# Performance work log

Measured on AMD Instinct MI355X. Metric: run time of the kernel, lower is better.

The kernel has to match this reference:

```python
import jax, jax.numpy as jnp
import numpy as np

N_NODES = 50000   # gnn_nodes_num
N_EDGES = 800000  # avg degree 16
HIDDEN = 64       # hidden_channels
BATCH_Y = 2048    # |y|


def setup_inputs() -> dict:
    key = jax.random.key(0)
    ks = jax.random.split(key, 16)
    s = 0.05
    H = HIDDEN
    return {
        "x": jnp.arange(N_NODES, dtype=jnp.int32),
        "edge_index": jax.random.randint(ks[0], (2, N_EDGES), 0, N_NODES, dtype=jnp.int32),
        "y": jax.random.randint(ks[1], (BATCH_Y,), 0, N_NODES, dtype=jnp.int32),
        # learned params
        "emb": jax.random.normal(ks[2], (N_NODES, H), dtype=jnp.float32) * s,
        "Wq": jax.random.normal(ks[3], (H, H), dtype=jnp.float32) * s,
        "bq": jnp.zeros((H,), dtype=jnp.float32),
        "Wk": jax.random.normal(ks[4], (H, H), dtype=jnp.float32) * s,
        "bk": jnp.zeros((H,), dtype=jnp.float32),
        "Wv": jax.random.normal(ks[5], (H, H), dtype=jnp.float32) * s,
        "bv": jnp.zeros((H,), dtype=jnp.float32),
        "Ws": jax.random.normal(ks[6], (H, H), dtype=jnp.float32) * s,  # root/skip lin
        "bs": jnp.zeros((H,), dtype=jnp.float32),
        "W1": jax.random.normal(ks[7], (H, N_NODES), dtype=jnp.float32) * s,
        "b1": jnp.zeros((N_NODES,), dtype=jnp.float32),
    }


def reference(x, edge_index, y, emb, Wq, bq, Wk, bk, Wv, bv, Ws, bs, W1, b1):
    H = Wq.shape[1]
    h = emb[x]                                  # [N, H] embedding lookup
    src, dst = edge_index[0], edge_index[1]

    # TransformerConv (heads=1, root_weight=True): per-node projections
    q = h @ Wq + bq                             # [N, H]
    k = h @ Wk + bk
    v = h @ Wv + bv

    # attention logits per edge, softmax grouped by destination node
    logits = jnp.sum(q[dst] * k[src], axis=-1) / jnp.sqrt(jnp.float32(H))  # [E]
    m = jax.ops.segment_max(logits, dst, num_segments=N_NODES)             # [N]
    e = jnp.exp(logits - m[dst])
    denom = jax.ops.segment_sum(e, dst, num_segments=N_NODES)              # [N]
    alpha = e / denom[dst]                                                 # [E]

    agg = jax.ops.segment_sum(alpha[:, None] * v[src], dst, num_segments=N_NODES)
    out = agg + h @ Ws + bs                     # [N, H] GAT output

    # for each node u: sum of out[dst] over edges with src == u  (vectorized
    # form of the original per-y boolean-mask loop), then gather at y
    neigh = jax.ops.segment_sum(out[dst], src, num_segments=N_NODES)       # [N, H]
    new_x = neigh[y]                            # [B, H]

    return jax.nn.softmax(new_x @ W1 + b1, axis=-1)  # [B, N]
```

## Files before the change

kernel.cpp:

```cpp
#include <hip/hip_runtime.h>
#include <math.h>

#define NN 50000
#define NE 800000
#define HH 64
#define NB 2048
#define NPAD 53248
#define NST3 52
#define TPS3 16
#define LOG2E 1.4426950408889634f
#define HBLK 3125
#define QBLK 782

typedef __attribute__((ext_vector_type(8))) short bf16x8;
typedef __attribute__((ext_vector_type(4))) float f32x4;

__device__ inline ushort f2bf(float f) {
  uint u = __float_as_uint(f);
  uint r = (u + 0x7fffu + ((u >> 16) & 1u)) >> 16;
  return (ushort)r;
}
__device__ inline float bf2f(uint u) { return __uint_as_float(u << 16); }

__device__ inline float fexp2(float x) {
#if __has_builtin(__builtin_amdgcn_exp2f)
  return __builtin_amdgcn_exp2f(x);
#else
  return exp2f(x);
#endif
}

__global__ __launch_bounds__(256) void k_prep(
    const float* __restrict__ W1, const float* __restrict__ b1,
    const float* __restrict__ Wq, const float* __restrict__ Wk,
    const float* __restrict__ Wv, const float* __restrict__ Ws,
    ushort* __restrict__ w1p, float* __restrict__ eb, ushort* __restrict__ WT,
    int* cnt_d, int* cnt_s, char* flag, char* ymark)
{
  int i = blockIdx.x * 256 + threadIdx.x;
  if (i < NN) { cnt_d[i] = 0; cnt_s[i] = 0; flag[i] = 0; ymark[i] = 0; }
  if (i < 4 * HH * HH) {
    int m = i >> 12, rem = i & 4095;
    int c = rem >> 6, kk = rem & 63;
    const float* W = (m == 0) ? Wq : (m == 1) ? Wk : (m == 2) ? Wv : Ws;
    WT[i] = f2bf(W[kk * HH + c]);
  }
  if (i < NPAD) {
    eb[i] = (i < NN) ? __expf(b1[i]) : 0.f;
    uint4 o[8];
    ushort* op = (ushort*)o;
    if (i < NN) {
#pragma unroll
      for (int k = 0; k < HH; ++k) op[k] = f2bf(W1[(size_t)k * NN + i] * LOG2E);
    } else {
#pragma unroll
      for (int k = 0; k < HH; ++k) op[k] = 0;
    }
    int t = i >> 6, nt = (i >> 4) & 3, lr = i & 15;
    ushort* tp = w1p + (size_t)t * 4096;
#pragma unroll
    for (int kt = 0; kt < 2; ++kt)
#pragma unroll
      for (int lk = 0; lk < 4; ++lk)
        *(uint4*)(tp + (kt * 4 + nt) * 512 + (lk * 16 + lr) * 8) = o[kt * 4 + lk];
  }
}

__global__ __launch_bounds__(256) void k_mark(const int* __restrict__ y,
                                              char* __restrict__ ymark) {
  int i = blockIdx.x * 256 + threadIdx.x;
  if (i < NB) ymark[y[i]] = 1;
}

__global__ __launch_bounds__(256) void k_hq(
    const int* __restrict__ src, const int* __restrict__ dst,
    const char* __restrict__ ymark,
    int* cnt_s, int* cnt_d, char* __restrict__ flag,
    int* __restrict__ rank_d, int* __restrict__ rank_s,
    const int* __restrict__ x, const float* __restrict__ emb,
    const ushort* __restrict__ WT,
    const float* __restrict__ bq, const float* __restrict__ bk,
    const float* __restrict__ bv, const float* __restrict__ bs,
    ushort* __restrict__ qb, ushort* __restrict__ kb, ushort* __restrict__ vb,
    float* __restrict__ hs)
{
  if (blockIdx.x < HBLK) {
    int e = blockIdx.x * 256 + threadIdx.x;
    if (e < NE) {
      int s = src[e], d = dst[e];
      rank_d[e] = atomicAdd(&cnt_d[d], 1);
      if (ymark[s]) {
        rank_s[e] = atomicAdd(&cnt_s[s], 1);
        flag[d] = 1;
      } else {
        rank_s[e] = -1;
      }
    }
    return;
  }
  int l = threadIdx.x & 63, w = threadIdx.x >> 6;
  int lr = l & 15, lk = l >> 4;
  int r0 = (blockIdx.x - HBLK) * 64;
  const ushort* wt = WT + w * HH * HH;
  const float* B = (w == 0) ? bq : (w == 1) ? bk : (w == 2) ? bv : bs;

  bf16x8 b[2][4];
#pragma unroll
  for (int kt = 0; kt < 2; ++kt)
#pragma unroll
    for (int nt = 0; nt < 4; ++nt)
      b[kt][nt] = *(const bf16x8*)(wt + (nt * 16 + lr) * HH + kt * 32 + lk * 8);

  bf16x8 a[2][4];
#pragma unroll
  for (int mt = 0; mt < 4; ++mt) {
    int row = r0 + mt * 16 + lr;
    int g = (row < NN) ? x[row] : 0;
    const float* hp = emb + (size_t)g * HH;
#pragma unroll
    for (int kt = 0; kt < 2; ++kt) {
      float4 f0 = *(const float4*)(hp + kt * 32 + lk * 8);
      float4 f1 = *(const float4*)(hp + kt * 32 + lk * 8 + 4);
      bf16x8 af;
      af[0] = f2bf(f0.x); af[1] = f2bf(f0.y); af[2] = f2bf(f0.z); af[3] = f2bf(f0.w);
      af[4] = f2bf(f1.x); af[5] = f2bf(f1.y); af[6] = f2bf(f1.z); af[7] = f2bf(f1.w);
      a[kt][mt] = af;
    }
  }

  f32x4 acc[4][4];
  const f32x4 z4 = {0.f, 0.f, 0.f, 0.f};
#pragma unroll
  for (int mt = 0; mt < 4; ++mt)
#pragma unroll
    for (int nt = 0; nt < 4; ++nt) acc[mt][nt] = z4;
#pragma unroll
  for (int kt = 0; kt < 2; ++kt)
#pragma unroll
    for (int mt = 0; mt < 4; ++mt)
#pragma unroll
      for (int nt = 0; nt < 4; ++nt)
        acc[mt][nt] = __builtin_amdgcn_mfma_f32_16x16x32_bf16(a[kt][mt], b[kt][nt], acc[mt][nt], 0, 0, 0);

  if (w < 3) {
    ushort* Db = (w == 0) ? qb : (w == 1) ? kb : vb;
#pragma unroll
    for (int mt = 0; mt < 4; ++mt)
#pragma unroll
      for (int r = 0; r < 4; ++r) {
        int row = r0 + mt * 16 + lk * 4 + r;
        if (row < NN) {
#pragma unroll
          for (int nt = 0; nt < 4; ++nt) {
            int c = nt * 16 + lr;
            Db[(size_t)row * HH + c] = f2bf(acc[mt][nt][r] + B[c]);
          }
        }
      }
  } else {
#pragma unroll
    for (int mt = 0; mt < 4; ++mt)
#pragma unroll
      for (int r = 0; r < 4; ++r) {
        int row = r0 + mt * 16 + lk * 4 + r;
        if (row < NN) {
#pragma unroll
          for (int nt = 0; nt < 4; ++nt) {
            int c = nt * 16 + lr;
            hs[(size_t)row * HH + c] = acc[mt][nt][r] + B[c];
          }
        }
      }
  }
}

__global__ __launch_bounds__(1024) void k_scan(
    const int* __restrict__ cnt_d, int* indptr_d,
    const int* __restrict__ cnt_s, int* indptr_s)
{
  const int* cnt = (blockIdx.x == 0) ? cnt_d : cnt_s;
  int* indptr    = (blockIdx.x == 0) ? indptr_d : indptr_s;
  __shared__ int sums[1024];
  const int CH = (NN + 1023) / 1024;
  int t = threadIdx.x;
  int begin = t * CH;
  int end = begin + CH; if (end > NN) end = NN;
  int s = 0;
  for (int i = begin; i < end; ++i) s += cnt[i];
  sums[t] = s;
  __syncthreads();
  for (int off = 1; off < 1024; off <<= 1) {
    int val = (t >= off) ? sums[t - off] : 0;
    __syncthreads();
    sums[t] += val;
    __syncthreads();
  }
  int prefix = (t == 0) ? 0 : sums[t - 1];
  for (int i = begin; i < end; ++i) {
    indptr[i] = prefix;
    prefix += cnt[i];
  }
  if (t == 0) indptr[NN] = sums[1023];
}

__global__ __launch_bounds__(256) void k_efill(
    const int* __restrict__ src, const int* __restrict__ dst,
    const ushort* __restrict__ qb, const ushort* __restrict__ kb,
    const char* __restrict__ flag,
    const int* __restrict__ indptr_s, const int* __restrict__ indptr_d,
    const int* __restrict__ rank_d, const int* __restrict__ rank_s,
    int* __restrict__ dstlist_s, int2* __restrict__ slot_d)
{
  int gid = blockIdx.x * 256 + threadIdx.x;
  int e = gid >> 2;
  int lane = gid & 3;
  if (e >= NE) return;
  int s = src[e], d = dst[e];
  bool fd = flag[d];
  float p = 0.f;
  if (fd) {
    const uint4* qp = (const uint4*)(qb + (size_t)d * HH + lane * 16);
    const uint4* kp = (const uint4*)(kb + (size_t)s * HH + lane * 16);
    uint4 qa0 = qp[0], ka0 = kp[0];
    uint4 qa1 = qp[1], ka1 = kp[1];
    p += bf2f(qa0.x & 0xffffu) * bf2f(ka0.x & 0xffffu) + bf2f(qa0.x >> 16) * bf2f(ka0.x >> 16);
    p += bf2f(qa0.y & 0xffffu) * bf2f(ka0.y & 0xffffu) + bf2f(qa0.y >> 16) * bf2f(ka0.y >> 16);
    p += bf2f(qa0.z & 0xffffu) * bf2f(ka0.z & 0xffffu) + bf2f(qa0.z >> 16) * bf2f(ka0.z >> 16);
    p += bf2f(qa0.w & 0xffffu) * bf2f(ka0.w & 0xffffu) + bf2f(qa0.w >> 16) * bf2f(ka0.w >> 16);
    p += bf2f(qa1.x & 0xffffu) * bf2f(ka1.x & 0xffffu) + bf2f(qa1.x >> 16) * bf2f(ka1.x >> 16);
    p += bf2f(qa1.y & 0xffffu) * bf2f(ka1.y & 0xffffu) + bf2f(qa1.y >> 16) * bf2f(ka1.y >> 16);
    p += bf2f(qa1.z & 0xffffu) * bf2f(ka1.z & 0xffffu) + bf2f(qa1.z >> 16) * bf2f(ka1.z >> 16);
    p += bf2f(qa1.w & 0xffffu) * bf2f(ka1.w & 0xffffu) + bf2f(qa1.w >> 16) * bf2f(ka1.w >> 16);
    p += __shfl_xor(p, 2);
    p += __shfl_xor(p, 1);
  }
  if (lane == 0) {
    if (fd) {
      int pd = indptr_d[d] + rank_d[e];
      int2 sl; sl.x = s; sl.y = __float_as_int(p * (0.125f * LOG2E));
      slot_d[pd] = sl;
    }
    int rs = rank_s[e];
    if (rs >= 0) dstlist_s[indptr_s[s] + rs] = d;
  }
}

__global__ __launch_bounds__(256) void k_agg(
    const int* __restrict__ indptr_d, const int2* __restrict__ slot_d,
    const ushort* __restrict__ vb, const char* __restrict__ flag,
    float* __restrict__ hs)
{
  int w = (blockIdx.x * 256 + threadIdx.x) >> 6;
  int lane = threadIdx.x & 63;
  if (w >= NN) return;
  if (!flag[w]) return;
  int beg = indptr_d[w], end = indptr_d[w + 1];
  if (beg == end) return;
  float den0 = 0.f, den1 = 0.f, acc0 = 0.f, acc1 = 0.f;
  int j = beg;
  for (; j + 1 < end; j += 2) {
    int2 sa = slot_d[j];
    int2 sb = slot_d[j + 1];
    float pa = fexp2(__int_as_float(sa.y));
    float pb = fexp2(__int_as_float(sb.y));
    float va = bf2f((uint)vb[(size_t)sa.x * HH + lane]);
    float vc = bf2f((uint)vb[(size_t)sb.x * HH + lane]);
    den0 += pa; den1 += pb;
    acc0 = fmaf(pa, va, acc0);
    acc1 = fmaf(pb, vc, acc1);
  }
  if (j < end) {
    int2 sa = slot_d[j];
    float pa = fexp2(__int_as_float(sa.y));
    den0 += pa;
    acc0 = fmaf(pa, bf2f((uint)vb[(size_t)sa.x * HH + lane]), acc0);
  }
  hs[(size_t)w * HH + lane] += (acc0 + acc1) / (den0 + den1);
}

__global__ __launch_bounds__(256) void k_newx(
    const int* __restrict__ y, const int* __restrict__ indptr_s,
    const int* __restrict__ dstlist_s, const float* __restrict__ outn,
    ushort* __restrict__ nxbf)
{
  int w = (blockIdx.x * 256 + threadIdx.x) >> 6;
  int lane = threadIdx.x & 63;
  if (w >= NB) return;
  int u = y[w];
  int beg = indptr_s[u], end = indptr_s[u + 1];
  float acc = 0.f;
  for (int j = beg; j < end; ++j) acc += outn[(size_t)dstlist_s[j] * HH + lane];
  nxbf[w * HH + lane] = f2bf(acc);
}

#define LOADP(A, t) do { const ushort* tp_ = w1p + (size_t)(t) * 4096;           \
  _Pragma("unroll") for (int kt = 0; kt < 2; ++kt)                               \
  _Pragma("unroll") for (int nt = 0; nt < 4; ++nt)                               \
    A[kt][nt] = *(const bf16x8*)(tp_ + (kt * 4 + nt) * 512 + l * 8);             \
} while (0)

#define MFMA8(A, acc) do {                                                       \
  _Pragma("unroll") for (int kt = 0; kt < 2; ++kt)                               \
  _Pragma("unroll") for (int nt = 0; nt < 4; ++nt)                               \
    acc[nt] = __builtin_amdgcn_mfma_f32_16x16x32_bf16(A[kt][nt], bm[kt], acc[nt], 0, 0, 0); \
} while (0)

__global__ __launch_bounds__(256) void k_finZ(
    const ushort* __restrict__ nxbf, const ushort* __restrict__ w1p,
    const float* __restrict__ eb, ushort* __restrict__ zb,
    float* __restrict__ Spart)
{
  __shared__ ushort lt[4][16][512];
  int tid = threadIdx.x;
  int l = tid & 63, w = tid >> 6;
  int lr = l & 15, lk = l >> 4;
  int b = blockIdx.x;
  int st = b % NST3, rg = b / NST3;
  int r0 = rg * 64 + w * 16;
  int tile0 = st * TPS3;
  const f32x4 z4 = {0.f, 0.f, 0.f, 0.f};

  bf16x8 bm[2];
#pragma unroll
  for (int kt = 0; kt < 2; ++kt)
    bm[kt] = *(const bf16x8*)(nxbf + (size_t)(r0 + lr) * HH + kt * 32 + lk * 8);

  float se = 0.f;
#pragma unroll
  for (int s = 0; s < 2; ++s) {
#pragma unroll
    for (int t = 0; t < 8; ++t) {
      int tile = tile0 + s * 8 + t;
      bf16x8 A0[2][4];
      LOADP(A0, tile);
      f32x4 acc[4];
#pragma unroll
      for (int nt = 0; nt < 4; ++nt) acc[nt] = z4;
      MFMA8(A0, acc);
#pragma unroll
      for (int nt = 0; nt < 4; ++nt) {
        int n0 = tile * 64 + nt * 16 + lk * 4;
        f32x4 e4 = *(const f32x4*)(eb + n0);
        union { _Float16 h[4]; uint2 u; } pk;
#pragma unroll
        for (int r = 0; r < 4; ++r) {
          float ur = fexp2(acc[nt][r]) * e4[r];
          se += ur;
          pk.h[r] = (_Float16)ur;
        }
        int uL = t * 16 + nt * 4 + lk;
        int uP = uL ^ (2 * (lr & 7));
        *(uint2*)&lt[w][lr][uP * 4] = pk.u;
      }
    }
    int colbase = (tile0 + s * 8) * 64;
#pragma unroll
    for (int r = 0; r < 16; ++r) {
      uint4 v = *(const uint4*)&lt[w][r][(l ^ (r & 7)) * 8];
      *(uint4*)(zb + (size_t)(r0 + r) * NPAD + colbase + l * 8) = v;
    }
  }
  se += __shfl_xor(se, 16);
  se += __shfl_xor(se, 32);
  if (lk == 0) Spart[(r0 + lr) * NST3 + st] = se;
}

__global__ __launch_bounds__(256) void k_sinv(const float* __restrict__ Spart,
                                              float* __restrict__ Sinv) {
  int r = blockIdx.x * 256 + threadIdx.x;
  if (r < NB) {
    float s = 0.f;
#pragma unroll
    for (int j = 0; j < NST3; ++j) s += Spart[r * NST3 + j];
    Sinv[r] = 1.0f / s;
  }
}

__global__ __launch_bounds__(256) void k_finN(
    const ushort* __restrict__ zb, const float* __restrict__ Sinv,
    float* __restrict__ out)
{
  int r = blockIdx.x;
  float sv = Sinv[r];
  const ushort* zr = zb + (size_t)r * NPAD;
  float* orow = out + (size_t)r * NN;
  for (int c0 = threadIdx.x * 8; c0 < NN; c0 += 2048) {
    uint4 zv = *(const uint4*)(zr + c0);
    const _Float16* hp = (const _Float16*)&zv;
    f32x4 v0, v1;
#pragma unroll
    for (int j = 0; j < 4; ++j) {
      v0[j] = (float)hp[j] * sv;
      v1[j] = (float)hp[4 + j] * sv;
    }
    *(f32x4*)(orow + c0) = v0;
    *(f32x4*)(orow + c0 + 4) = v1;
  }
}

#define PROCA(A, t) do { int bn0_ = (t) * 64;                                    \
  f32x4 acc[4];                                                                  \
  _Pragma("unroll") for (int nt = 0; nt < 4; ++nt) acc[nt] = z4;                 \
  MFMA8(A, acc);                                                                 \
  _Pragma("unroll") for (int nt = 0; nt < 4; ++nt) {                             \
    int n0 = bn0_ + nt * 16 + lk * 4;                                            \
    f32x4 e4 = *(const f32x4*)(eb + n0);                                         \
    _Pragma("unroll") for (int r = 0; r < 4; ++r)                                \
      se += fexp2(acc[nt][r]) * e4[r];                                           \
  }                                                                              \
} while (0)

#define PROCB(A, t) do { int bn0_ = (t) * 64;                                    \
  f32x4 acc[4];                                                                  \
  _Pragma("unroll") for (int nt = 0; nt < 4; ++nt) acc[nt] = z4;                 \
  MFMA8(A, acc);                                                                 \
  _Pragma("unroll") for (int nt = 0; nt < 4; ++nt) {                             \
    int n0 = bn0_ + nt * 16 + lk * 4;                                            \
    f32x4 e4 = *(const f32x4*)(eb + n0);                                         \
    f32x4 vx;                                                                    \
    _Pragma("unroll") for (int r = 0; r < 4; ++r)                                \
      vx[r] = fexp2(acc[nt][r]) * e4[r] * sv;                                    \
    if (n0 < NN)                                                                 \
      __builtin_nontemporal_store(vx, (f32x4*)(out + (size_t)(r0 + lr) * NN + n0)); \
  }                                                                              \
} while (0)

__global__ __launch_bounds__(256, 4) void k_finA(
    const ushort* __restrict__ nxbf, const ushort* __restrict__ w1p,
    const float* __restrict__ eb, float* __restrict__ Spart)
{
  int tid = threadIdx.x;
  int l = tid & 63, w = tid >> 6;
  int lr = l & 15, lk = l >> 4;
  int b = blockIdx.x;
  int st = b % NST3, rg = b / NST3;
  int r0 = rg * 64 + w * 16;
  int tile0 = st * TPS3;
  const f32x4 z4 = {0.f, 0.f, 0.f, 0.f};
  bf16x8 bm[2];
#pragma unroll
  for (int kt = 0; kt < 2; ++kt)
    bm[kt] = *(const bf16x8*)(nxbf + (size_t)(r0 + lr) * HH + kt * 32 + lk * 8);
  float se = 0.f;
  {
    bf16x8 A0[2][4];
#pragma unroll
    for (int t = 0; t < TPS3; ++t) { LOADP(A0, tile0 + t); PROCA(A0, tile0 + t); }
  }
  se += __shfl_xor(se, 16);
  se += __shfl_xor(se, 32);
  if (lk == 0) Spart[(r0 + lr) * NST3 + st] = se;
}

__global__ __launch_bounds__(256, 4) void k_finB(
    const ushort* __restrict__ nxbf, const ushort* __restrict__ w1p,
    const float* __restrict__ eb, const float* __restrict__ Sinv,
    float* __restrict__ out)
{
  int tid = threadIdx.x;
  int l = tid & 63, w = tid >> 6;
  int lr = l & 15, lk = l >> 4;
  int b = blockIdx.x;
  int st = b % NST3, rg = b / NST3;
  int r0 = rg * 64 + w * 16;
  int tile0 = st * TPS3;
  const f32x4 z4 = {0.f, 0.f, 0.f, 0.f};
  bf16x8 bm[2];
#pragma unroll
  for (int kt = 0; kt < 2; ++kt)
    bm[kt] = *(const bf16x8*)(nxbf + (size_t)(r0 + lr) * HH + kt * 32 + lk * 8);
  float sv = Sinv[r0 + lr];
  {
    bf16x8 A0[2][4];
#pragma unroll
    for (int t = 0; t < TPS3; ++t) { LOADP(A0, tile0 + t); PROCB(A0, tile0 + t); }
  }
}

extern "C" void kernel_launch(void* const* d_in, const int* in_sizes, int n_in,
                              void* d_out, int out_size, void* d_ws, size_t ws_size,
                              hipStream_t stream)
{
  const int* x   = (const int*)d_in[0];
  const int* src = (const int*)d_in[1];
  const int* dst = src + NE;
  const int* y   = (const int*)d_in[2];
  const float* emb = (const float*)d_in[3];
  const float* Wq = (const float*)d_in[4];  const float* bq = (const float*)d_in[5];
  const float* Wk = (const float*)d_in[6];  const float* bk = (const float*)d_in[7];
  const float* Wv = (const float*)d_in[8];  const float* bv = (const float*)d_in[9];
  const float* Ws = (const float*)d_in[10]; const float* bs = (const float*)d_in[11];
  const float* W1 = (const float*)d_in[12]; const float* b1 = (const float*)d_in[13];
  float* out = (float*)d_out;

  char* wsb = (char*)d_ws;
  ushort* nxbf  = (ushort*)wsb;
  ushort* w1p   = (ushort*)(wsb + 262144);
  float*  Spart = (float*)(wsb + 7077888);
  float*  Sinv  = (float*)(wsb + 7503872);
  float*  eb    = (float*)(wsb + 7512064);
  const size_t PERS   = 7725056;
  const size_t ZSZ    = (size_t)NB * NPAD * 2;
  const size_t PERS_Z = PERS + ZSZ;
  const size_t BIGSZ  = 46400000;
  bool zpath = ws_size >= PERS_Z + BIGSZ;
  ushort* zb = (ushort*)(wsb + PERS);
  char* big = zpath ? (wsb + PERS_Z)
                    : ((ws_size >= PERS + BIGSZ) ? (wsb + PERS) : (char*)d_out);
  ushort* qb     = (ushort*)(big + 0);
  ushort* kb     = (ushort*)(big + 6400000);
  ushort* vb     = (ushort*)(big + 12800000);
  float*  hs     = (float*)(big + 19200000);
  int2*   slot_d = (int2*)(big + 32000000);
  int* dstlist_s = (int*)(big + 38400000);
  int* rank_d    = (int*)(big + 38700000);
  int* rank_s    = (int*)(big + 41900000);
  int* cnt_d     = (int*)(big + 45100000);
  int* cnt_s     = (int*)(big + 45300000);
  int* indptr_d  = (int*)(big + 45500000);
  int* indptr_s  = (int*)(big + 45700064);
  char* flag     = (char*)(big + 45900128);
  char* ymark    = (char*)(big + 45950176);
  ushort* WT     = (ushort*)(big + 46000224);

  k_prep<<<dim3(224), dim3(256), 0, stream>>>(W1, b1, Wq, Wk, Wv, Ws, w1p, eb, WT,
                                              cnt_d, cnt_s, flag, ymark);
  k_mark<<<dim3(8), dim3(256), 0, stream>>>(y, ymark);
  k_hq<<<dim3(HBLK + QBLK), dim3(256), 0, stream>>>(src, dst, ymark,
                                                    cnt_s, cnt_d, flag, rank_d, rank_s,
                                                    x, emb, WT, bq, bk, bv, bs,
                                                    qb, kb, vb, hs);
  k_scan<<<dim3(2), dim3(1024), 0, stream>>>(cnt_d, indptr_d, cnt_s, indptr_s);
  k_efill<<<dim3(12500), dim3(256), 0, stream>>>(src, dst, qb, kb, flag,
                                                 indptr_s, indptr_d, rank_d, rank_s,
                                                 dstlist_s, slot_d);
  k_agg<<<dim3(12500), dim3(256), 0, stream>>>(indptr_d, slot_d, vb, flag, hs);
  k_newx<<<dim3(512), dim3(256), 0, stream>>>(y, indptr_s, dstlist_s, hs, nxbf);
  if (zpath) {
    k_finZ<<<dim3(NST3 * 32), dim3(256), 0, stream>>>(nxbf, w1p, eb, zb, Spart);
    k_sinv<<<dim3(8), dim3(256), 0, stream>>>(Spart, Sinv);
    k_finN<<<dim3(NB), dim3(256), 0, stream>>>(zb, Sinv, out);
  } else {
    k_finA<<<dim3(NST3 * 32), dim3(256), 0, stream>>>(nxbf, w1p, eb, Spart);
    k_sinv<<<dim3(8), dim3(256), 0, stream>>>(Spart, Sinv);
    k_finB<<<dim3(NST3 * 32), dim3(256), 0, stream>>>(nxbf, w1p, eb, Sinv, out);
  }
}
```

Baseline: 439.9 us.

## Repartition final GEMM into 64 strips with double-buffered W1 loads and swizzled block order

Splits the output columns into 64 strips of 13 tiles instead of 52 strips of 16, giving a grid of 2048 blocks. The block index is remapped so consecutive blocks land on different strips, which may change L2 and channel locality. In k_finZ, W1 tiles are now double-buffered so the next tile loads while the current one is processed. The LDS staging buffer is halved and flushed every 4 tiles with narrower stores, and the last tile is written straight to global memory. The trade-off is more register pressure and smaller, less coalesced z-buffer stores.

```diff
diff --git a/kernel.cpp b/kernel.cpp
--- a/kernel.cpp
+++ b/kernel.cpp
@@ -6,8 +6,8 @@
 #define HH 64
 #define NB 2048
 #define NPAD 53248
-#define NST3 52
-#define TPS3 16
+#define NST4 64
+#define TPS4 13
 #define LOG2E 1.4426950408889634f
 #define HBLK 3125
 #define QBLK 782
@@ -305,19 +305,39 @@
     acc[nt] = __builtin_amdgcn_mfma_f32_16x16x32_bf16(A[kt][nt], bm[kt], acc[nt], 0, 0, 0); \
 } while (0)
 
+#define PROCZ(A, tile, tt) do {                                                  \
+  f32x4 acc[4];                                                                  \
+  _Pragma("unroll") for (int nt = 0; nt < 4; ++nt) acc[nt] = z4;                 \
+  MFMA8(A, acc);                                                                 \
+  _Pragma("unroll") for (int nt = 0; nt < 4; ++nt) {                             \
+    int n0 = (tile) * 64 + nt * 16 + lk * 4;                                     \
+    f32x4 e4 = *(const f32x4*)(eb + n0);                                         \
+    union { _Float16 h[4]; uint u2[2]; } pk;                                     \
+    _Pragma("unroll") for (int r = 0; r < 4; ++r) {                              \
+      float ur = fexp2(acc[nt][r]) * e4[r];                                      \
+      se += ur;                                                                  \
+      pk.h[r] = (_Float16)ur;                                                    \
+    }                                                                            \
+    int uL = (tt) * 16 + nt * 4 + lk;                                            \
+    int uP = uL ^ ((lr & 7) << 3);                                               \
+    *(uint2*)&lt[w][lr][uP * 4] = *(uint2*)pk.u2;                                \
+  }                                                                              \
+} while (0)
+
 __global__ __launch_bounds__(256) void k_finZ(
     const ushort* __restrict__ nxbf, const ushort* __restrict__ w1p,
     const float* __restrict__ eb, ushort* __restrict__ zb,
     float* __restrict__ Spart)
 {
-  __shared__ ushort lt[4][16][512];
+  __shared__ ushort lt[4][16][256];
   int tid = threadIdx.x;
   int l = tid & 63, w = tid >> 6;
   int lr = l & 15, lk = l >> 4;
   int b = blockIdx.x;
-  int st = b % NST3, rg = b / NST3;
+  int st = (b & 7) * 8 + ((b >> 3) & 7);
+  int rg = b >> 6;
   int r0 = rg * 64 + w * 16;
-  int tile0 = st * TPS3;
+  int tile0 = st * TPS4;
   const f32x4 z4 = {0.f, 0.f, 0.f, 0.f};
 
   bf16x8 bm[2];
@@ -326,43 +346,51 @@
     bm[kt] = *(const bf16x8*)(nxbf + (size_t)(r0 + lr) * HH + kt * 32 + lk * 8);
 
   float se = 0.f;
-#pragma unroll
-  for (int s = 0; s < 2; ++s) {
-#pragma unroll
-    for (int t = 0; t < 8; ++t) {
-      int tile = tile0 + s * 8 + t;
-      bf16x8 A0[2][4];
-      LOADP(A0, tile);
-      f32x4 acc[4];
-#pragma unroll
-      for (int nt = 0; nt < 4; ++nt) acc[nt] = z4;
-      MFMA8(A0, acc);
-#pragma unroll
-      for (int nt = 0; nt < 4; ++nt) {
-        int n0 = tile * 64 + nt * 16 + lk * 4;
-        f32x4 e4 = *(const f32x4*)(eb + n0);
-        union { _Float16 h[4]; uint2 u; } pk;
-#pragma unroll
-        for (int r = 0; r < 4; ++r) {
-          float ur = fexp2(acc[nt][r]) * e4[r];
-          se += ur;
-          pk.h[r] = (_Float16)ur;
-        }
-        int uL = t * 16 + nt * 4 + lk;
-        int uP = uL ^ (2 * (lr & 7));
-        *(uint2*)&lt[w][lr][uP * 4] = pk.u;
+  bf16x8 A0[2][4], A1[2][4];
+  LOADP(A0, tile0);
+#pragma unroll
+  for (int s = 0; s < 3; ++s) {
+#pragma unroll
+    for (int tt = 0; tt < 4; ++tt) {
+      int tile = tile0 + s * 4 + tt;
+      if (tt & 1) {
+        if (tile + 1 <= tile0 + 12) LOADP(A0, tile + 1);
+        PROCZ(A1, tile, tt);
+      } else {
+        LOADP(A1, tile + 1);
+        PROCZ(A0, tile, tt);
       }
     }
-    int colbase = (tile0 + s * 8) * 64;
+    int colbase = (tile0 + s * 4) * 64;
 #pragma unroll
     for (int r = 0; r < 16; ++r) {
-      uint4 v = *(const uint4*)&lt[w][r][(l ^ (r & 7)) * 8];
-      *(uint4*)(zb + (size_t)(r0 + r) * NPAD + colbase + l * 8) = v;
+      uint2 v = *(const uint2*)&lt[w][r][(l ^ ((r & 7) << 3)) * 4];
+      *(uint2*)(zb + (size_t)(r0 + r) * NPAD + colbase + l * 4) = v;
+    }
+  }
+  {
+    int tile = tile0 + 12;
+    f32x4 acc[4];
+#pragma unroll
+    for (int nt = 0; nt < 4; ++nt) acc[nt] = z4;
+    MFMA8(A0, acc);
+#pragma unroll
+    for (int nt = 0; nt < 4; ++nt) {
+      int n0 = tile * 64 + nt * 16 + lk * 4;
+      f32x4 e4 = *(const f32x4*)(eb + n0);
+      union { _Float16 h[4]; uint u2[2]; } pk;
+#pragma unroll
+      for (int r = 0; r < 4; ++r) {
+        float ur = fexp2(acc[nt][r]) * e4[r];
+        se += ur;
+        pk.h[r] = (_Float16)ur;
+      }
+      *(uint2*)(zb + (size_t)(r0 + lr) * NPAD + n0) = *(uint2*)pk.u2;
     }
   }
   se += __shfl_xor(se, 16);
   se += __shfl_xor(se, 32);
-  if (lk == 0) Spart[(r0 + lr) * NST3 + st] = se;
+  if (lk == 0) Spart[(r0 + lr) * NST4 + st] = se;
 }
 
 __global__ __launch_bounds__(256) void k_sinv(const float* __restrict__ Spart,
@@ -371,7 +399,7 @@
   if (r < NB) {
     float s = 0.f;
 #pragma unroll
-    for (int j = 0; j < NST3; ++j) s += Spart[r * NST3 + j];
+    for (int j = 0; j < NST4; ++j) s += Spart[r * NST4 + j];
     Sinv[r] = 1.0f / s;
   }
 }
@@ -433,9 +461,10 @@
   int l = tid & 63, w = tid >> 6;
   int lr = l & 15, lk = l >> 4;
   int b = blockIdx.x;
-  int st = b % NST3, rg = b / NST3;
+  int st = (b & 7) * 8 + ((b >> 3) & 7);
+  int rg = b >> 6;
   int r0 = rg * 64 + w * 16;
-  int tile0 = st * TPS3;
+  int tile0 = st * TPS4;
   const f32x4 z4 = {0.f, 0.f, 0.f, 0.f};
   bf16x8 bm[2];
 #pragma unroll
@@ -445,11 +474,11 @@
   {
     bf16x8 A0[2][4];
 #pragma unroll
-    for (int t = 0; t < TPS3; ++t) { LOADP(A0, tile0 + t); PROCA(A0, tile0 + t); }
+    for (int t = 0; t < TPS4; ++t) { LOADP(A0, tile0 + t); PROCA(A0, tile0 + t); }
   }
   se += __shfl_xor(se, 16);
   se += __shfl_xor(se, 32);
-  if (lk == 0) Spart[(r0 + lr) * NST3 + st] = se;
+  if (lk == 0) Spart[(r0 + lr) * NST4 + st] = se;
 }
 
 __global__ __launch_bounds__(256, 4) void k_finB(
@@ -461,9 +490,10 @@
   int l = tid & 63, w = tid >> 6;
   int lr = l & 15, lk = l >> 4;
   int b = blockIdx.x;
-  int st = b % NST3, rg = b / NST3;
+  int st = (b & 7) * 8 + ((b >> 3) & 7);
+  int rg = b >> 6;
   int r0 = rg * 64 + w * 16;
-  int tile0 = st * TPS3;
+  int tile0 = st * TPS4;
   const f32x4 z4 = {0.f, 0.f, 0.f, 0.f};
   bf16x8 bm[2];
 #pragma unroll
@@ -473,7 +503,7 @@
   {
     bf16x8 A0[2][4];
 #pragma unroll
-    for (int t = 0; t < TPS3; ++t) { LOADP(A0, tile0 + t); PROCB(A0, tile0 + t); }
+    for (int t = 0; t < TPS4; ++t) { LOADP(A0, tile0 + t); PROCB(A0, tile0 + t); }
   }
 }
 
@@ -497,9 +527,9 @@
   ushort* nxbf  = (ushort*)wsb;
   ushort* w1p   = (ushort*)(wsb + 262144);
   float*  Spart = (float*)(wsb + 7077888);
-  float*  Sinv  = (float*)(wsb + 7503872);
-  float*  eb    = (float*)(wsb + 7512064);
-  const size_t PERS   = 7725056;
+  float*  Sinv  = (float*)(wsb + 7602176);
+  float*  eb    = (float*)(wsb + 7610368);
+  const size_t PERS   = 7823360;
   const size_t ZSZ    = (size_t)NB * NPAD * 2;
   const size_t PERS_Z = PERS + ZSZ;
   const size_t BIGSZ  = 46400000;
@@ -537,12 +567,12 @@
   k_agg<<<dim3(12500), dim3(256), 0, stream>>>(indptr_d, slot_d, vb, flag, hs);
   k_newx<<<dim3(512), dim3(256), 0, stream>>>(y, indptr_s, dstlist_s, hs, nxbf);
   if (zpath) {
-    k_finZ<<<dim3(NST3 * 32), dim3(256), 0, stream>>>(nxbf, w1p, eb, zb, Spart);
+    k_finZ<<<dim3(2048), dim3(256), 0, stream>>>(nxbf, w1p, eb, zb, Spart);
     k_sinv<<<dim3(8), dim3(256), 0, stream>>>(Spart, Sinv);
     k_finN<<<dim3(NB), dim3(256), 0, stream>>>(zb, Sinv, out);
   } else {
-    k_finA<<<dim3(NST3 * 32), dim3(256), 0, stream>>>(nxbf, w1p, eb, Spart);
+    k_finA<<<dim3(2048), dim3(256), 0, stream>>>(nxbf, w1p, eb, Spart);
     k_sinv<<<dim3(8), dim3(256), 0, stream>>>(Spart, Sinv);
-    k_finB<<<dim3(NST3 * 32), dim3(256), 0, stream>>>(nxbf, w1p, eb, Sinv, out);
-  }
-}
+    k_finB<<<dim3(2048), dim3(256), 0, stream>>>(nxbf, w1p, eb, Sinv, out);
+  }
+}
```

New measurement: 460.5 us. +4.7%, slower.
